# Kernel tuning notes

Measured on AMD Instinct MI355X. Metric: run time of the kernel, lower is better.

The kernel has to match this reference:

```python
import jax, jax.numpy as jnp
import numpy as np

HEADS = 16
KV_HEADS = 8
HEAD_DIM = 128
ROPE_BASE = 10000.0
RMS_EPS = 1e-5


def rmsnorm(x, w, eps=RMS_EPS):
    x = jnp.clip(x.astype(jnp.float32), -100.0, 100.0)
    var = jnp.clip(jnp.mean(x * x, axis=-1, keepdims=True), eps, None)
    x = x * jax.lax.rsqrt(var + eps)
    x = jnp.clip(x, -10.0, 10.0)
    return w * x


def activation_quant(x):
    x = jnp.clip(x, -50.0, 50.0)
    max_val = jnp.clip(jnp.max(jnp.abs(x), axis=-1, keepdims=True), 0.0001, None)
    scale = 127.0 / max_val
    return jnp.clip(jnp.round(x * scale), -128.0, 127.0) / scale


def weight_quant(w):
    scale = jnp.clip(jnp.mean(jnp.abs(w)), 1e-8, None)
    e = jnp.mean(w)
    return jnp.sign(w - e) * scale


def bitlinear(x, w, norm_w):
    xn = rmsnorm(x, norm_w)
    xq = xn + jax.lax.stop_gradient(activation_quant(xn) - xn)
    wq = w + jax.lax.stop_gradient(weight_quant(w) - w)
    return xq @ wq.T


def rope_tables(seq_len, dim):
    inv_freq = 1.0 / (ROPE_BASE ** (jnp.arange(0, dim, 2, dtype=jnp.float32) / dim))
    freqs = jnp.outer(jnp.arange(seq_len, dtype=jnp.float32), inv_freq)  # [S, dim/2]
    emb = jnp.concatenate([freqs, freqs], axis=-1)  # [S, dim]
    return jnp.cos(emb), jnp.sin(emb)


def rotate_half(x):
    x1, x2 = jnp.split(x, 2, axis=-1)
    return jnp.concatenate([-x2, x1], axis=-1)


def attention_forward(hidden_states, attention_mask, wq, wk, wv, wo, nq, nk, nv, no):
    B, S, H = hidden_states.shape
    q = bitlinear(hidden_states, wq, nq)  # [B,S,nh*hd]
    k = bitlinear(hidden_states, wk, nk)  # [B,S,nkv*hd]
    v = bitlinear(hidden_states, wv, nv)

    q = q.reshape(B, S, HEADS, HEAD_DIM).transpose(0, 2, 1, 3)       # [B,nh,S,hd]
    k = k.reshape(B, S, KV_HEADS, HEAD_DIM).transpose(0, 2, 1, 3)    # [B,nkv,S,hd]
    v = v.reshape(B, S, KV_HEADS, HEAD_DIM).transpose(0, 2, 1, 3)

    cos, sin = rope_tables(S, HEAD_DIM)
    cos = cos[None, None]  # [1,1,S,hd]
    sin = sin[None, None]
    q = q * cos + rotate_half(q) * sin
    k = k * cos + rotate_half(k) * sin

    groups = HEADS // KV_HEADS
    k_exp = jnp.repeat(k, groups, axis=1)  # [B,nh,S,hd]
    v_exp = jnp.repeat(v, groups, axis=1)

    scale = 1.0 / jnp.sqrt(jnp.float32(HEAD_DIM))
    scores = jnp.einsum('bhqd,bhkd->bhqk', q, k_exp) * scale
    scores = scores + attention_mask
    attn = jax.nn.softmax(scores, axis=-1)
    out = jnp.einsum('bhqk,bhkd->bhqd', attn, v_exp)
    out = out.transpose(0, 2, 1, 3).reshape(B, S, HEADS * HEAD_DIM)
    return bitlinear(out, wo, no)


def setup_inputs() -> dict:
    key = jax.random.key(0)
    ks = jax.random.split(key, 6)
    B, S, H = 2, 2048, 2048
    KVH = KV_HEADS * HEAD_DIM
    std = 0.02 / np.sqrt(H)
    return {
        'hidden_states': jax.random.normal(ks[0], (B, S, H), jnp.float32),
        'attention_mask': jnp.zeros((1, 1, S, S), jnp.float32),
        'wq': jax.random.normal(ks[1], (H, H), jnp.float32) * std,
        'wk': jax.random.normal(ks[2], (KVH, H), jnp.float32) * std,
        'wv': jax.random.normal(ks[3], (KVH, H), jnp.float32) * std,
        'wo': jax.random.normal(ks[4], (H, H), jnp.float32) * std,
        'nq': jnp.ones((H,), jnp.float32),
        'nk': jnp.ones((H,), jnp.float32),
        'nv': jnp.ones((H,), jnp.float32),
        'no': jnp.ones((H,), jnp.float32),
    }


def reference(hidden_states, attention_mask, wq, wk, wv, wo, nq, nk, nv, no):
    return attention_forward(hidden_states, attention_mask, wq, wk, wv, wo, nq, nk, nv, no)
```

## Files before the change

kernel.cpp:

```cpp
#include <hip/hip_runtime.h>


#define DI __device__ __forceinline__

using bf16   = __bf16;
using bf16x4 = __attribute__((ext_vector_type(4))) __bf16;
using bf16x8 = __attribute__((ext_vector_type(8))) __bf16;
using f32x4  = __attribute__((ext_vector_type(4))) float;

DI void gl_lds16(void* lds, const void* g) {
  __builtin_amdgcn_global_load_lds((const __attribute__((address_space(1))) void*)g,
                                   (__attribute__((address_space(3))) void*)lds, 16, 0, 0);
}
DI float clampf(float x, float lo, float hi) { return fminf(fmaxf(x, lo), hi); }

DI float block_sum(float v, float* red, int lane, int w) {
#pragma unroll
  for (int o = 32; o > 0; o >>= 1) v += __shfl_xor(v, o, 64);
  __syncthreads();
  if (lane == 0) red[w] = v;
  __syncthreads();
  return red[0] + red[1] + red[2] + red[3];
}
DI float block_max(float v, float* red, int lane, int w) {
#pragma unroll
  for (int o = 32; o > 0; o >>= 1) v = fmaxf(v, __shfl_xor(v, o, 64));
  __syncthreads();
  if (lane == 0) red[w] = v;
  __syncthreads();
  return fmaxf(fmaxf(red[0], red[1]), fmaxf(red[2], red[3]));
}

__global__ void wstats_kernel(const float* wq, const float* wk, const float* wv,
                              const float* wo, float* stats) {
  __shared__ float red[4], red2[4];
  int t = threadIdx.x, lane = t & 63, w = t >> 6;
  int m = blockIdx.y;
  const float* src; int n4;
  if (m == 0)      { src = wq; n4 = 1048576; }
  else if (m == 1) { src = wk; n4 = 524288;  }
  else if (m == 2) { src = wv; n4 = 524288;  }
  else             { src = wo; n4 = 1048576; }
  float s = 0.f, sa = 0.f;
  for (int i = blockIdx.x * 256 + t; i < n4; i += 256 * 256) {
    float4 v = ((const float4*)src)[i];
    s  += v.x + v.y + v.z + v.w;
    sa += fabsf(v.x) + fabsf(v.y) + fabsf(v.z) + fabsf(v.w);
  }
#pragma unroll
  for (int o = 32; o > 0; o >>= 1) { s += __shfl_xor(s, o, 64); sa += __shfl_xor(sa, o, 64); }
  if (lane == 0) { red[w] = s; red2[w] = sa; }
  __syncthreads();
  if (t == 0) {
    atomicAdd(&stats[2 * m],     red[0] + red[1] + red[2] + red[3]);
    atomicAdd(&stats[2 * m + 1], red2[0] + red2[1] + red2[2] + red2[3]);
  }
}

__global__ void wsign_kernel(const float* wq, const float* wk, const float* wv, const float* wo,
                             ushort* sq, ushort* sk, ushort* sv, ushort* so,
                             const float* stats) {
  int m = blockIdx.y;
  const float* src; ushort* dst; int n4; float cinv;
  if (m == 0)      { src = wq; dst = sq; n4 = 1048576; cinv = 1.f / 4194304.f; }
  else if (m == 1) { src = wk; dst = sk; n4 = 524288;  cinv = 1.f / 2097152.f; }
  else if (m == 2) { src = wv; dst = sv; n4 = 524288;  cinv = 1.f / 2097152.f; }
  else             { src = wo; dst = so; n4 = 1048576; cinv = 1.f / 4194304.f; }
  float e = stats[2 * m] * cinv;
  for (int i = blockIdx.x * 256 + threadIdx.x; i < n4; i += 1024 * 256) {
    float4 v = ((const float4*)src)[i];
    ushort4 o;
    o.x = v.x > e ? 0x3F80 : (v.x < e ? 0xBF80 : 0);
    o.y = v.y > e ? 0x3F80 : (v.y < e ? 0xBF80 : 0);
    o.z = v.z > e ? 0x3F80 : (v.z < e ? 0xBF80 : 0);
    o.w = v.w > e ? 0x3F80 : (v.w < e ? 0xBF80 : 0);
    ((ushort4*)dst)[i] = o;
  }
}

__global__ void ropetab_kernel(float* ct, float* st) {
  int s = blockIdx.x, j = threadIdx.x;
  float invf = powf(10000.f, -(float)j * (1.f / 64.f));
  float a = (float)s * invf;
  ct[s * 64 + j] = cosf(a);
  st[s * 64 + j] = sinf(a);
}

DI void quant_one(const float* xs, const float* __restrict__ wt, bf16* __restrict__ a,
                  float* __restrict__ r, int row, int t, int lane, int w, float* red) {
  float4 w0 = ((const float4*)wt)[t * 2], w1 = ((const float4*)wt)[t * 2 + 1];
  float wv[8] = {w0.x, w0.y, w0.z, w0.w, w1.x, w1.y, w1.z, w1.w};
  float y[8]; float am = 0.f;
#pragma unroll
  for (int e = 0; e < 8; ++e) {
    y[e] = clampf(wv[e] * xs[e], -50.f, 50.f);
    am = fmaxf(am, fabsf(y[e]));
  }
  float mx = block_max(am, red, lane, w);
  float maxval = fmaxf(mx, 1e-4f);
  float sc = 127.f / maxval;
  bf16x8 q;
#pragma unroll
  for (int e = 0; e < 8; ++e) {
    float n = rintf(y[e] * sc);
    n = clampf(n, -128.f, 127.f);
    q[e] = (bf16)n;
  }
  *(bf16x8*)(a + (size_t)row * 2048 + t * 8) = q;
  if (t == 0) r[row] = maxval * (1.f / 127.f);
}

template <int NW>
__launch_bounds__(256)
__global__ void rqnorm_kernel(const float* __restrict__ x,
                              const float* __restrict__ w0, const float* __restrict__ w1,
                              const float* __restrict__ w2,
                              bf16* a0, bf16* a1, bf16* a2,
                              float* r0, float* r1, float* r2) {
  __shared__ float red[4];
  int t = threadIdx.x, lane = t & 63, w = t >> 6;
  int row = blockIdx.x;
  const float* xr = x + (size_t)row * 2048;
  float4 u0 = ((const float4*)xr)[t * 2], u1 = ((const float4*)xr)[t * 2 + 1];
  float xs[8] = {u0.x, u0.y, u0.z, u0.w, u1.x, u1.y, u1.z, u1.w};
  float ss = 0.f;
#pragma unroll
  for (int e = 0; e < 8; ++e) { xs[e] = clampf(xs[e], -100.f, 100.f); ss += xs[e] * xs[e]; }
  float tot = block_sum(ss, red, lane, w);
  float var = fmaxf(tot * (1.f / 2048.f), 1e-5f);
  float inv = 1.f / sqrtf(var + 1e-5f);
#pragma unroll
  for (int e = 0; e < 8; ++e) xs[e] = clampf(xs[e] * inv, -10.f, 10.f);
  quant_one(xs, w0, a0, r0, row, t, lane, w, red);
  if (NW > 1) quant_one(xs, w1, a1, r1, row, t, lane, w, red);
  if (NW > 2) quant_one(xs, w2, a2, r2, row, t, lane, w, red);
}

DI void mm_core(const bf16* __restrict__ Ag0, const bf16* __restrict__ Bg0,
                bf16* As, bf16* Bs, int w, int lane, f32x4 acc[2][8]) {
  int l15 = lane & 15, quad = lane >> 4;
  int srow = w * 8 + (lane >> 3);
  int sc_p = (lane & 7) * 8;
  int sc_g = ((lane & 7) ^ (lane >> 3)) * 8;
  const bf16* Ag = Ag0 + (size_t)srow * 2048 + sc_g;
  const bf16* Bg = Bg0 + (size_t)srow * 2048 + sc_g;
  bf16* Al = As + srow * 64 + sc_p;
  bf16* Bl = Bs + srow * 64 + sc_p;
  for (int kt = 0; kt < 32; ++kt) {
    size_t kb = (size_t)kt * 64;
#pragma unroll
    for (int i = 0; i < 4; ++i) {
      gl_lds16(Al + i * 32 * 64, Ag + (size_t)i * 32 * 2048 + kb);
      gl_lds16(Bl + i * 32 * 64, Bg + (size_t)i * 32 * 2048 + kb);
    }
    __syncthreads();
#pragma unroll
    for (int kc = 0; kc < 2; ++kc) {
      bf16x8 af[2], bfr[8];
#pragma unroll
      for (int mt = 0; mt < 2; ++mt)
        af[mt] = *(const bf16x8*)(As + (w * 32 + mt * 16 + l15) * 64 +
                                  (((kc * 4 + quad) ^ (l15 & 7)) * 8));
#pragma unroll
      for (int nt = 0; nt < 8; ++nt)
        bfr[nt] = *(const bf16x8*)(Bs + (nt * 16 + l15) * 64 +
                                   (((kc * 4 + quad) ^ (l15 & 7)) * 8));
#pragma unroll
      for (int mt = 0; mt < 2; ++mt)
#pragma unroll
        for (int nt = 0; nt < 8; ++nt)
          acc[mt][nt] = __builtin_amdgcn_mfma_f32_16x16x32_bf16(af[mt], bfr[nt], acc[mt][nt], 0, 0, 0);
    }
    __syncthreads();
  }
}

__launch_bounds__(256, 2)
__global__ void qkv_gemm(const bf16* __restrict__ Aq, const bf16* __restrict__ Ak,
                         const bf16* __restrict__ Av, const bf16* __restrict__ Ball,
                         const float* __restrict__ rq, const float* __restrict__ rk,
                         const float* __restrict__ rv, const float* __restrict__ stats,
                         bf16* __restrict__ qr, bf16* __restrict__ kr,
                         float* __restrict__ vlin,
                         const float* __restrict__ ct, const float* __restrict__ st) {
  __shared__ bf16 As[128 * 64];
  __shared__ bf16 Bs[128 * 64];
  int t = threadIdx.x, w = t >> 6, lane = t & 63;
  int l15 = lane & 15, quad = lane >> 4;
  int x = blockIdx.x, m0 = blockIdx.y * 128;
  const bf16* A; const float* rs; float sw; int brow0;
  if (x < 16)      { A = Aq; rs = rq; sw = stats[1] * (1.f / 4194304.f); brow0 = x * 128; }
  else if (x < 24) { A = Ak; rs = rk; sw = stats[3] * (1.f / 2097152.f); brow0 = 2048 + (x - 16) * 128; }
  else             { A = Av; rs = rv; sw = stats[5] * (1.f / 2097152.f); brow0 = 3072 + (x - 24) * 128; }
  sw = fmaxf(sw, 1e-8f);
  f32x4 acc[2][8] = {};
  mm_core(A + (size_t)m0 * 2048, Ball + (size_t)brow0 * 2048, As, Bs, w, lane, acc);

  if (x < 24) {
    constexpr float QROPE = 0.08838834764831845f * 1.4426950408889634f;
    float qmul = (x < 16) ? QROPE : 1.f;
    bf16* outb = (x < 16) ? qr : kr;
    int h = (x < 16) ? x : x - 16;
    int nh = (x < 16) ? 16 : 8;
#pragma unroll
    for (int mt = 0; mt < 2; ++mt)
#pragma unroll
      for (int r = 0; r < 4; ++r) {
        int row = m0 + w * 32 + mt * 16 + quad * 4 + r;
        float rsc = rs[row] * sw * qmul;
        int s = row & 2047, b = row >> 11;
        size_t base = ((size_t)(b * nh + h) * 2048 + s) * 128;
#pragma unroll
        for (int nt = 0; nt < 4; ++nt) {
          int d = nt * 16 + l15;
          float x1 = acc[mt][nt][r] * rsc;
          float x2 = acc[mt][nt + 4][r] * rsc;
          float c = ct[s * 64 + d], sn = st[s * 64 + d];
          outb[base + d]      = (bf16)(x1 * c - x2 * sn);
          outb[base + d + 64] = (bf16)(x2 * c + x1 * sn);
        }
      }
  } else {
    int n0 = (x - 24) * 128;
#pragma unroll
    for (int mt = 0; mt < 2; ++mt)
#pragma unroll
      for (int r = 0; r < 4; ++r) {
        int row = m0 + w * 32 + mt * 16 + quad * 4 + r;
        float rsc = rs[row] * sw;
#pragma unroll
        for (int nt = 0; nt < 8; ++nt)
          vlin[(size_t)row * 1024 + n0 + nt * 16 + l15] = acc[mt][nt][r] * rsc;
      }
  }
}

__launch_bounds__(256, 2)
__global__ void gemm_o(const bf16* __restrict__ A, const bf16* __restrict__ Bw,
                       const float* __restrict__ rs, const float* __restrict__ stats,
                       float* __restrict__ out) {
  __shared__ bf16 As[128 * 64];
  __shared__ bf16 Bs[128 * 64];
  int t = threadIdx.x, w = t >> 6, lane = t & 63;
  int l15 = lane & 15, quad = lane >> 4;
  int m0 = blockIdx.y * 128, n0 = blockIdx.x * 128;
  f32x4 acc[2][8] = {};
  mm_core(A + (size_t)m0 * 2048, Bw + (size_t)n0 * 2048, As, Bs, w, lane, acc);
  float sw = fmaxf(stats[7] * (1.f / 4194304.f), 1e-8f);
#pragma unroll
  for (int mt = 0; mt < 2; ++mt)
#pragma unroll
    for (int r = 0; r < 4; ++r) {
      int row = m0 + w * 32 + mt * 16 + quad * 4 + r;
      float rsc = rs[row] * sw;
#pragma unroll
      for (int nt = 0; nt < 8; ++nt)
        out[(size_t)row * 2048 + n0 + nt * 16 + l15] = acc[mt][nt][r] * rsc;
    }
}

__global__ void vtrans_kernel(const float* __restrict__ v_lin, bf16* __restrict__ v_t) {
  __shared__ float tile[64][65];
  int t = threadIdx.x, c = t & 63, rq = t >> 6;
  int ct0 = blockIdx.x * 64, tt0 = blockIdx.y * 64;
#pragma unroll
  for (int i = 0; i < 16; ++i) {
    int r = rq * 16 + i;
    tile[r][c] = v_lin[(size_t)(tt0 + r) * 1024 + ct0 + c];
  }
  __syncthreads();
  int token = tt0 + c;
  int b = token >> 11, s = token & 2047;
#pragma unroll
  for (int i = 0; i < 16; ++i) {
    int cg = ct0 + rq * 16 + i;
    int kvh = cg >> 7, d = cg & 127;
    v_t[((size_t)(b * 8 + kvh) * 128 + d) * 2048 + s] = (bf16)tile[c][rq * 16 + i];
  }
}

__launch_bounds__(512, 4)
__global__ void attn_kernel(const bf16* __restrict__ Q, const bf16* __restrict__ Kc,
                            const bf16* __restrict__ Vt, const float* __restrict__ mask,
                            float* __restrict__ Oout) {
  constexpr float L2E  = 1.4426950408889634f;
  constexpr float DTHR = 8.f * L2E;
  __shared__ bf16 Ks[2][64 * 128];
  __shared__ bf16 Vs[2][128 * 64];
  __shared__ bf16 Ps[128 * 64];
  int t = threadIdx.x, w = t >> 6, lane = t & 63;
  int l15 = lane & 15, quad = lane >> 4;
  int bh = blockIdx.y, b = bh >> 4, h = bh & 15, kvh = h >> 1;
  int q0 = blockIdx.x * 128;
  const bf16* Qb = Q + (size_t)(b * 16 + h) * 2048 * 128;
  const bf16* Kb = Kc + (size_t)(b * 8 + kvh) * 2048 * 128;
  const bf16* Vb = Vt + (size_t)(b * 8 + kvh) * 128 * 2048;

  int qloc = w * 16 + l15;
  int qg = q0 + qloc;

  bf16x8 qf[4];
#pragma unroll
  for (int kc = 0; kc < 4; ++kc)
    qf[kc] = *(const bf16x8*)(Qb + (size_t)qg * 128 + kc * 32 + quad * 8);

  f32x4 Oa[8] = {};
  float mrow = -1e30f, lrow = 0.f;

  auto stage = [&](int buf, int kt) {
    int kk0 = kt * 64;
#pragma unroll
    for (int i = 0; i < 2; ++i) {
      int c = t + i * 512;
      int kr = c >> 4, c16 = c & 15;
      gl_lds16(&Ks[buf][c * 8],
               Kb + (size_t)(kk0 + kr) * 128 + ((c16 ^ (kr & 15)) * 8));
    }
#pragma unroll
    for (int i = 0; i < 2; ++i) {
      int c = t + i * 512;
      int vr = c >> 3, c8 = c & 7;
      gl_lds16(&Vs[buf][c * 8],
               Vb + (size_t)vr * 2048 + kk0 + ((c8 ^ (vr & 7)) * 8));
    }
  };

  stage(0, 0);

  f32x4 mv[4];
#pragma unroll
  for (int k2 = 0; k2 < 4; ++k2)
    mv[k2] = *(const f32x4*)(mask + (size_t)qg * 2048 + k2 * 16 + quad * 4);

  for (int kt = 0; kt < 32; ++kt) {
    int cur = kt & 1;
    __syncthreads();
    if (kt < 31) stage(cur ^ 1, kt + 1);

    f32x4 Sacc[4] = {};
    __builtin_amdgcn_s_setprio(1);
#pragma unroll
    for (int kc = 0; kc < 4; ++kc) {
      bf16x8 kf[4];
#pragma unroll
      for (int k2 = 0; k2 < 4; ++k2)
        kf[k2] = *(const bf16x8*)(&Ks[cur][(k2 * 16 + l15) * 128 + (((kc * 4 + quad) ^ l15) * 8)]);
#pragma unroll
      for (int k2 = 0; k2 < 4; ++k2)
        Sacc[k2] = __builtin_amdgcn_mfma_f32_16x16x32_bf16(kf[k2], qf[kc], Sacc[k2], 0, 0, 0);
    }
    __builtin_amdgcn_s_setprio(0);

#pragma unroll
    for (int k2 = 0; k2 < 4; ++k2)
#pragma unroll
      for (int r = 0; r < 4; ++r)
        Sacc[k2][r] = fmaf(mv[k2][r], L2E, Sacc[k2][r]);
    f32x4 vm;
#pragma unroll
    for (int r = 0; r < 4; ++r)
      vm[r] = fmaxf(fmaxf(Sacc[0][r], Sacc[1][r]), fmaxf(Sacc[2][r], Sacc[3][r]));
    float mx = fmaxf(fmaxf(vm[0], vm[1]), fmaxf(vm[2], vm[3]));
    mx = fmaxf(mx, __shfl_xor(mx, 16, 64));
    mx = fmaxf(mx, __shfl_xor(mx, 32, 64));
    if (!__all(mx <= mrow + DTHR)) {
      float mnew = fmaxf(mrow, mx);
      float alpha = exp2f(mrow - mnew);
      mrow = mnew;
      lrow *= alpha;
#pragma unroll
      for (int dt = 0; dt < 8; ++dt) Oa[dt] *= alpha;
    }
    f32x4 vs = {0.f, 0.f, 0.f, 0.f};
#pragma unroll
    for (int k2 = 0; k2 < 4; ++k2) {
      bf16x4 pk;
#pragma unroll
      for (int r = 0; r < 4; ++r) {
        float p = exp2f(Sacc[k2][r] - mrow);
        vs[r] += p;
        pk[r] = (bf16)p;
      }
      int c = k2 * 2 + (quad >> 1);
      *(bf16x4*)(&Ps[qloc * 64 + ((c ^ (qloc & 7)) * 8) + (quad & 1) * 4]) = pk;
    }
    float rsum = (vs[0] + vs[1]) + (vs[2] + vs[3]);
    rsum += __shfl_xor(rsum, 16, 64);
    rsum += __shfl_xor(rsum, 32, 64);
    lrow += rsum;

    if (kt < 31) {
      int kk1 = (kt + 1) * 64;
#pragma unroll
      for (int k2 = 0; k2 < 4; ++k2)
        mv[k2] = *(const f32x4*)(mask + (size_t)qg * 2048 + kk1 + k2 * 16 + quad * 4);
    }

    __builtin_amdgcn_s_setprio(1);
#pragma unroll
    for (int kc = 0; kc < 2; ++kc) {
      bf16x8 pf = *(const bf16x8*)(&Ps[qloc * 64 + (((kc * 4 + quad) ^ (l15 & 7)) * 8)]);
#pragma unroll
      for (int dt = 0; dt < 8; ++dt) {
        bf16x8 vf = *(const bf16x8*)(&Vs[cur][(dt * 16 + l15) * 64 +
                                              (((kc * 4 + quad) ^ (l15 & 7)) * 8)]);
        Oa[dt] = __builtin_amdgcn_mfma_f32_16x16x32_bf16(vf, pf, Oa[dt], 0, 0, 0);
      }
    }
    __builtin_amdgcn_s_setprio(0);
  }

  float inv = 1.f / lrow;
  int token = b * 2048 + qg;
#pragma unroll
  for (int dt = 0; dt < 8; ++dt) {
    f32x4 o = Oa[dt] * inv;
    *(f32x4*)(Oout + (size_t)token * 2048 + h * 128 + dt * 16 + quad * 4) = o;
  }
}

extern "C" void kernel_launch(void* const* d_in, const int* in_sizes, int n_in,
                              void* d_out, int out_size, void* d_ws, size_t ws_size,
                              hipStream_t stream) {
  const float* hidden = (const float*)d_in[0];
  const float* mask   = (const float*)d_in[1];
  const float* wq = (const float*)d_in[2];
  const float* wk = (const float*)d_in[3];
  const float* wv = (const float*)d_in[4];
  const float* wo = (const float*)d_in[5];
  const float* nq = (const float*)d_in[6];
  const float* nk = (const float*)d_in[7];
  const float* nv = (const float*)d_in[8];
  const float* no = (const float*)d_in[9];
  float* out = (float*)d_out;
  char* ws = (char*)d_ws;

  constexpr size_t O_STATS = 0;
  constexpr size_t O_CT    = 256;
  constexpr size_t O_ST    = O_CT + 524288;
  constexpr size_t O_SQ    = O_ST + 524288;
  constexpr size_t O_SK    = O_SQ + 8388608;
  constexpr size_t O_SV    = O_SK + 4194304;
  constexpr size_t O_SO    = O_SV + 4194304;
  constexpr size_t O_RSQ   = O_SO + 8388608;
  constexpr size_t O_RSK   = O_RSQ + 16384;
  constexpr size_t O_RSV   = O_RSK + 16384;
  constexpr size_t O_RSO   = O_RSV + 16384;
  constexpr size_t O_AQQ   = O_RSO + 16384;
  constexpr size_t O_AQK   = O_AQQ + 16777216;
  constexpr size_t O_AQV   = O_AQK + 16777216;
  constexpr size_t O_QR    = O_AQV + 16777216;
  constexpr size_t O_KR    = O_QR + 16777216;
  constexpr size_t O_VT    = O_KR + 8388608;
  constexpr size_t O_VLIN2 = O_VT + 8388608;
  constexpr size_t O_ATTN  = O_AQQ;
  constexpr size_t O_AQO   = O_AQV;

  float* stats = (float*)(ws + O_STATS);
  float* ct = (float*)(ws + O_CT);
  float* st = (float*)(ws + O_ST);

  (void)hipMemsetAsync(ws + O_STATS, 0, 256, stream);

  wstats_kernel<<<dim3(256, 4), 256, 0, stream>>>(wq, wk, wv, wo, stats);
  wsign_kernel<<<dim3(1024, 4), 256, 0, stream>>>(wq, wk, wv, wo,
      (ushort*)(ws + O_SQ), (ushort*)(ws + O_SK), (ushort*)(ws + O_SV), (ushort*)(ws + O_SO), stats);
  ropetab_kernel<<<dim3(2048), 64, 0, stream>>>(ct, st);

  rqnorm_kernel<3><<<dim3(4096), 256, 0, stream>>>(hidden, nq, nk, nv,
      (bf16*)(ws + O_AQQ), (bf16*)(ws + O_AQK), (bf16*)(ws + O_AQV),
      (float*)(ws + O_RSQ), (float*)(ws + O_RSK), (float*)(ws + O_RSV));

  qkv_gemm<<<dim3(32, 32), 256, 0, stream>>>(
      (const bf16*)(ws + O_AQQ), (const bf16*)(ws + O_AQK), (const bf16*)(ws + O_AQV),
      (const bf16*)(ws + O_SQ),
      (const float*)(ws + O_RSQ), (const float*)(ws + O_RSK), (const float*)(ws + O_RSV),
      stats, (bf16*)(ws + O_QR), (bf16*)(ws + O_KR), (float*)(ws + O_VLIN2), ct, st);

  vtrans_kernel<<<dim3(16, 64), 256, 0, stream>>>((const float*)(ws + O_VLIN2), (bf16*)(ws + O_VT));

  attn_kernel<<<dim3(16, 32), 512, 0, stream>>>(
      (const bf16*)(ws + O_QR), (const bf16*)(ws + O_KR), (const bf16*)(ws + O_VT),
      mask, (float*)(ws + O_ATTN));

  rqnorm_kernel<1><<<dim3(4096), 256, 0, stream>>>((const float*)(ws + O_ATTN), no, no, no,
      (bf16*)(ws + O_AQO), (bf16*)(ws + O_AQO), (bf16*)(ws + O_AQO),
      (float*)(ws + O_RSO), (float*)(ws + O_RSO), (float*)(ws + O_RSO));

  gemm_o<<<dim3(16, 32), 256, 0, stream>>>(
      (const bf16*)(ws + O_AQO), (const bf16*)(ws + O_SO), (float*)(ws + O_RSO), stats, out);

  (void)in_sizes; (void)n_in; (void)out_size; (void)ws_size;
}
```

Before: 424.2 us.

## Double-buffer GEMM LDS, fuse V transpose into QKV GEMM, batch quant reductions

The GEMM mainloop now keeps two LDS buffers and prefetches the next K-tile while computing the current one, so each iteration needs one barrier instead of two. The V projection epilogue transposes through LDS and writes bf16 V^T directly, which removes the fp32 intermediate buffer and the separate transpose kernel. The three per-matrix max reductions in the norm/quant kernel are batched into one shuffle pass and a single barrier. Both GEMMs also remap block IDs so that neighbouring blocks share operand tiles in cache. The cost is doubled LDS per GEMM block, which may reduce occupancy at the requested two blocks per CU.

After: 423.8 us. Within noise of the previous version (-0.1%).

```diff
diff --git a/kernel.cpp b/kernel.cpp
--- a/kernel.cpp
+++ b/kernel.cpp
@@ -21,14 +21,6 @@
   if (lane == 0) red[w] = v;
   __syncthreads();
   return red[0] + red[1] + red[2] + red[3];
-}
-DI float block_max(float v, float* red, int lane, int w) {
-#pragma unroll
-  for (int o = 32; o > 0; o >>= 1) v = fmaxf(v, __shfl_xor(v, o, 64));
-  __syncthreads();
-  if (lane == 0) red[w] = v;
-  __syncthreads();
-  return fmaxf(fmaxf(red[0], red[1]), fmaxf(red[2], red[3]));
 }
 
 __global__ void wstats_kernel(const float* wq, const float* wk, const float* wv,
@@ -86,30 +78,6 @@
   st[s * 64 + j] = sinf(a);
 }
 
-DI void quant_one(const float* xs, const float* __restrict__ wt, bf16* __restrict__ a,
-                  float* __restrict__ r, int row, int t, int lane, int w, float* red) {
-  float4 w0 = ((const float4*)wt)[t * 2], w1 = ((const float4*)wt)[t * 2 + 1];
-  float wv[8] = {w0.x, w0.y, w0.z, w0.w, w1.x, w1.y, w1.z, w1.w};
-  float y[8]; float am = 0.f;
-#pragma unroll
-  for (int e = 0; e < 8; ++e) {
-    y[e] = clampf(wv[e] * xs[e], -50.f, 50.f);
-    am = fmaxf(am, fabsf(y[e]));
-  }
-  float mx = block_max(am, red, lane, w);
-  float maxval = fmaxf(mx, 1e-4f);
-  float sc = 127.f / maxval;
-  bf16x8 q;
-#pragma unroll
-  for (int e = 0; e < 8; ++e) {
-    float n = rintf(y[e] * sc);
-    n = clampf(n, -128.f, 127.f);
-    q[e] = (bf16)n;
-  }
-  *(bf16x8*)(a + (size_t)row * 2048 + t * 8) = q;
-  if (t == 0) r[row] = maxval * (1.f / 127.f);
-}
-
 template <int NW>
 __launch_bounds__(256)
 __global__ void rqnorm_kernel(const float* __restrict__ x,
@@ -118,6 +86,7 @@
                               bf16* a0, bf16* a1, bf16* a2,
                               float* r0, float* r1, float* r2) {
   __shared__ float red[4];
+  __shared__ float redm[4][NW];
   int t = threadIdx.x, lane = t & 63, w = t >> 6;
   int row = blockIdx.x;
   const float* xr = x + (size_t)row * 2048;
@@ -131,9 +100,42 @@
   float inv = 1.f / sqrtf(var + 1e-5f);
 #pragma unroll
   for (int e = 0; e < 8; ++e) xs[e] = clampf(xs[e] * inv, -10.f, 10.f);
-  quant_one(xs, w0, a0, r0, row, t, lane, w, red);
-  if (NW > 1) quant_one(xs, w1, a1, r1, row, t, lane, w, red);
-  if (NW > 2) quant_one(xs, w2, a2, r2, row, t, lane, w, red);
+
+  float y[NW][8], am[NW];
+#pragma unroll
+  for (int m = 0; m < NW; ++m) {
+    const float* wt = (m == 0) ? w0 : (m == 1) ? w1 : w2;
+    float4 b0 = ((const float4*)wt)[t * 2], b1 = ((const float4*)wt)[t * 2 + 1];
+    float wv[8] = {b0.x, b0.y, b0.z, b0.w, b1.x, b1.y, b1.z, b1.w};
+    am[m] = 0.f;
+#pragma unroll
+    for (int e = 0; e < 8; ++e) {
+      y[m][e] = clampf(wv[e] * xs[e], -50.f, 50.f);
+      am[m] = fmaxf(am[m], fabsf(y[m][e]));
+    }
+  }
+#pragma unroll
+  for (int o = 32; o > 0; o >>= 1)
+#pragma unroll
+    for (int m = 0; m < NW; ++m) am[m] = fmaxf(am[m], __shfl_xor(am[m], o, 64));
+  if (lane == 0)
+#pragma unroll
+    for (int m = 0; m < NW; ++m) redm[w][m] = am[m];
+  __syncthreads();
+#pragma unroll
+  for (int m = 0; m < NW; ++m) {
+    bf16* a = (m == 0) ? a0 : (m == 1) ? a1 : a2;
+    float* r = (m == 0) ? r0 : (m == 1) ? r1 : r2;
+    float mx = fmaxf(fmaxf(redm[0][m], redm[1][m]), fmaxf(redm[2][m], redm[3][m]));
+    float maxval = fmaxf(mx, 1e-4f);
+    float sc = 127.f / maxval;
+    bf16x8 q;
+#pragma unroll
+    for (int e = 0; e < 8; ++e)
+      q[e] = (bf16)clampf(rintf(y[m][e] * sc), -128.f, 127.f);
+    *(bf16x8*)(a + (size_t)row * 2048 + t * 8) = q;
+    if (t == 0) r[row] = maxval * (1.f / 127.f);
+  }
 }
 
 DI void mm_core(const bf16* __restrict__ Ag0, const bf16* __restrict__ Bg0,
@@ -146,24 +148,32 @@
   const bf16* Bg = Bg0 + (size_t)srow * 2048 + sc_g;
   bf16* Al = As + srow * 64 + sc_p;
   bf16* Bl = Bs + srow * 64 + sc_p;
+  auto stage = [&](int buf, int kt) {
+    size_t kb = (size_t)kt * 64;
+    int lo = buf * 8192;
+#pragma unroll
+    for (int i = 0; i < 4; ++i) {
+      gl_lds16(Al + lo + i * 32 * 64, Ag + (size_t)i * 32 * 2048 + kb);
+      gl_lds16(Bl + lo + i * 32 * 64, Bg + (size_t)i * 32 * 2048 + kb);
+    }
+  };
+  stage(0, 0);
   for (int kt = 0; kt < 32; ++kt) {
-    size_t kb = (size_t)kt * 64;
-#pragma unroll
-    for (int i = 0; i < 4; ++i) {
-      gl_lds16(Al + i * 32 * 64, Ag + (size_t)i * 32 * 2048 + kb);
-      gl_lds16(Bl + i * 32 * 64, Bg + (size_t)i * 32 * 2048 + kb);
-    }
+    int cur = kt & 1;
     __syncthreads();
+    if (kt < 31) stage(cur ^ 1, kt + 1);
+    const bf16* Ac = As + cur * 8192;
+    const bf16* Bc = Bs + cur * 8192;
 #pragma unroll
     for (int kc = 0; kc < 2; ++kc) {
       bf16x8 af[2], bfr[8];
 #pragma unroll
       for (int mt = 0; mt < 2; ++mt)
-        af[mt] = *(const bf16x8*)(As + (w * 32 + mt * 16 + l15) * 64 +
+        af[mt] = *(const bf16x8*)(Ac + (w * 32 + mt * 16 + l15) * 64 +
                                   (((kc * 4 + quad) ^ (l15 & 7)) * 8));
 #pragma unroll
       for (int nt = 0; nt < 8; ++nt)
-        bfr[nt] = *(const bf16x8*)(Bs + (nt * 16 + l15) * 64 +
+        bfr[nt] = *(const bf16x8*)(Bc + (nt * 16 + l15) * 64 +
                                    (((kc * 4 + quad) ^ (l15 & 7)) * 8));
 #pragma unroll
       for (int mt = 0; mt < 2; ++mt)
@@ -171,7 +181,6 @@
         for (int nt = 0; nt < 8; ++nt)
           acc[mt][nt] = __builtin_amdgcn_mfma_f32_16x16x32_bf16(af[mt], bfr[nt], acc[mt][nt], 0, 0, 0);
     }
-    __syncthreads();
   }
 }
 
@@ -181,13 +190,15 @@
                          const float* __restrict__ rq, const float* __restrict__ rk,
                          const float* __restrict__ rv, const float* __restrict__ stats,
                          bf16* __restrict__ qr, bf16* __restrict__ kr,
-                         float* __restrict__ vlin,
+                         bf16* __restrict__ vt,
                          const float* __restrict__ ct, const float* __restrict__ st) {
-  __shared__ bf16 As[128 * 64];
-  __shared__ bf16 Bs[128 * 64];
+  __shared__ bf16 As[2 * 128 * 64];
+  __shared__ bf16 Bs[2 * 128 * 64];
   int t = threadIdx.x, w = t >> 6, lane = t & 63;
   int l15 = lane & 15, quad = lane >> 4;
-  int x = blockIdx.x, m0 = blockIdx.y * 128;
+  int bid = blockIdx.y * 32 + blockIdx.x;
+  bid = (bid & 7) * 128 + (bid >> 3);
+  int x = bid & 31, m0 = (bid >> 5) * 128;
   const bf16* A; const float* rs; float sw; int brow0;
   if (x < 16)      { A = Aq; rs = rq; sw = stats[1] * (1.f / 4194304.f); brow0 = x * 128; }
   else if (x < 24) { A = Ak; rs = rk; sw = stats[3] * (1.f / 2097152.f); brow0 = 2048 + (x - 16) * 128; }
@@ -221,17 +232,31 @@
         }
       }
   } else {
-    int n0 = (x - 24) * 128;
+    int kvh = x - 24;
+    bf16* tile = As;
+    __syncthreads();
 #pragma unroll
     for (int mt = 0; mt < 2; ++mt)
 #pragma unroll
       for (int r = 0; r < 4; ++r) {
-        int row = m0 + w * 32 + mt * 16 + quad * 4 + r;
-        float rsc = rs[row] * sw;
-#pragma unroll
-        for (int nt = 0; nt < 8; ++nt)
-          vlin[(size_t)row * 1024 + n0 + nt * 16 + l15] = acc[mt][nt][r] * rsc;
+        int tok = w * 32 + mt * 16 + quad * 4 + r;
+        float rsc = rs[m0 + tok] * sw;
+#pragma unroll
+        for (int nt = 0; nt < 8; ++nt) {
+          int f = nt * 16 + l15;
+          tile[f * 128 + (tok ^ ((f & 7) << 3))] = (bf16)(acc[mt][nt][r] * rsc);
+        }
       }
+    __syncthreads();
+    int f = t >> 1, tok0 = (t & 1) * 64;
+    int btok = m0 >> 11, s0 = m0 & 2047;
+    bf16* dst = vt + ((size_t)(btok * 8 + kvh) * 128 + f) * 2048 + s0 + tok0;
+    int sxor = (f & 7) << 3;
+#pragma unroll
+    for (int j = 0; j < 8; ++j) {
+      bf16x8 vv = *(const bf16x8*)(tile + f * 128 + ((tok0 + j * 8) ^ sxor));
+      *(bf16x8*)(dst + j * 8) = vv;
+    }
   }
 }
 
@@ -239,11 +264,13 @@
 __global__ void gemm_o(const bf16* __restrict__ A, const bf16* __restrict__ Bw,
                        const float* __restrict__ rs, const float* __restrict__ stats,
                        float* __restrict__ out) {
-  __shared__ bf16 As[128 * 64];
-  __shared__ bf16 Bs[128 * 64];
+  __shared__ bf16 As[2 * 128 * 64];
+  __shared__ bf16 Bs[2 * 128 * 64];
   int t = threadIdx.x, w = t >> 6, lane = t & 63;
   int l15 = lane & 15, quad = lane >> 4;
-  int m0 = blockIdx.y * 128, n0 = blockIdx.x * 128;
+  int bid = blockIdx.y * 16 + blockIdx.x;
+  bid = (bid & 7) * 64 + (bid >> 3);
+  int n0 = (bid & 15) * 128, m0 = (bid >> 4) * 128;
   f32x4 acc[2][8] = {};
   mm_core(A + (size_t)m0 * 2048, Bw + (size_t)n0 * 2048, As, Bs, w, lane, acc);
   float sw = fmaxf(stats[7] * (1.f / 4194304.f), 1e-8f);
@@ -257,26 +284,6 @@
       for (int nt = 0; nt < 8; ++nt)
         out[(size_t)row * 2048 + n0 + nt * 16 + l15] = acc[mt][nt][r] * rsc;
     }
-}
-
-__global__ void vtrans_kernel(const float* __restrict__ v_lin, bf16* __restrict__ v_t) {
-  __shared__ float tile[64][65];
-  int t = threadIdx.x, c = t & 63, rq = t >> 6;
-  int ct0 = blockIdx.x * 64, tt0 = blockIdx.y * 64;
-#pragma unroll
-  for (int i = 0; i < 16; ++i) {
-    int r = rq * 16 + i;
-    tile[r][c] = v_lin[(size_t)(tt0 + r) * 1024 + ct0 + c];
-  }
-  __syncthreads();
-  int token = tt0 + c;
-  int b = token >> 11, s = token & 2047;
-#pragma unroll
-  for (int i = 0; i < 16; ++i) {
-    int cg = ct0 + rq * 16 + i;
-    int kvh = cg >> 7, d = cg & 127;
-    v_t[((size_t)(b * 8 + kvh) * 128 + d) * 2048 + s] = (bf16)tile[c][rq * 16 + i];
-  }
 }
 
 __launch_bounds__(512, 4)
@@ -452,7 +459,6 @@
   constexpr size_t O_QR    = O_AQV + 16777216;
   constexpr size_t O_KR    = O_QR + 16777216;
   constexpr size_t O_VT    = O_KR + 8388608;
-  constexpr size_t O_VLIN2 = O_VT + 8388608;
   constexpr size_t O_ATTN  = O_AQQ;
   constexpr size_t O_AQO   = O_AQV;
 
@@ -475,9 +481,7 @@
       (const bf16*)(ws + O_AQQ), (const bf16*)(ws + O_AQK), (const bf16*)(ws + O_AQV),
       (const bf16*)(ws + O_SQ),
       (const float*)(ws + O_RSQ), (const float*)(ws + O_RSK), (const float*)(ws + O_RSV),
-      stats, (bf16*)(ws + O_QR), (bf16*)(ws + O_KR), (float*)(ws + O_VLIN2), ct, st);
-
-  vtrans_kernel<<<dim3(16, 64), 256, 0, stream>>>((const float*)(ws + O_VLIN2), (bf16*)(ws + O_VT));
+      stats, (bf16*)(ws + O_QR), (bf16*)(ws + O_KR), (bf16*)(ws + O_VT), ct, st);
 
   attn_kernel<<<dim3(16, 32), 512, 0, stream>>>(
       (const bf16*)(ws + O_QR), (const bf16*)(ws + O_KR), (const bf16*)(ws + O_VT),
```
